# Optimization experiments

Hardware: AMD Instinct MI355X
Metric: run time of the kernel (lower is better)

## Reference

```python
import jax, jax.numpy as jnp
import numpy as np

N_G, N_U, E, C = 100000, 100000, 3200000, 2000000


def graph_conv(x, edges, W_rel, W_root, b):
    # PyG GraphConv (aggr='add'): out_i = (sum_{j->i} x_j) @ W_rel + x_i @ W_root + b
    src, dst = edges[0], edges[1]
    agg = jax.ops.segment_sum(x[src], dst, num_segments=x.shape[0])
    return agg @ W_rel + x @ W_root + b


def setup_inputs() -> dict:
    key = jax.random.key(0)
    ks = jax.random.split(key, 16)
    d = {
        'x_u': jax.random.normal(ks[0], (N_U, 4), jnp.float32),
        'x_g': jax.random.normal(ks[1], (N_G, 4), jnp.float32),
        'candidates': jax.random.randint(ks[2], (C, 2), 0, N_G + N_U, jnp.int64),
        'edges': jax.random.randint(ks[3], (2, E), 0, N_G, jnp.int64),
        # GraphConv(4,8)
        'W1_rel': jax.random.normal(ks[4], (4, 8), jnp.float32) * 0.5,
        'W1_root': jax.random.normal(ks[5], (4, 8), jnp.float32) * 0.5,
        'b1': jax.random.normal(ks[6], (8,), jnp.float32) * 0.1,
        # GraphConv(8,16)
        'W2_rel': jax.random.normal(ks[7], (8, 16), jnp.float32) * 0.35,
        'W2_root': jax.random.normal(ks[8], (8, 16), jnp.float32) * 0.35,
        'b2': jax.random.normal(ks[9], (16,), jnp.float32) * 0.1,
        # fc_unconnected: Linear(4,16) (Dropout is identity in eval)
        'W_un': jax.random.normal(ks[10], (4, 16), jnp.float32) * 0.5,
        'b_un': jax.random.normal(ks[11], (16,), jnp.float32) * 0.1,
        # fc: Linear(32,64) -> SELU -> Linear(64,1)
        'W_fc1': jax.random.normal(ks[12], (32, 64), jnp.float32) * 0.18,
        'b_fc1': jax.random.normal(ks[13], (64,), jnp.float32) * 0.1,
        'W_fc2': jax.random.normal(ks[14], (64, 1), jnp.float32) * 0.12,
        'b_fc2': jax.random.normal(ks[15], (1,), jnp.float32) * 0.1,
    }
    return d


def reference(x_u, x_g, candidates, edges,
              W1_rel, W1_root, b1, W2_rel, W2_root, b2,
              W_un, b_un, W_fc1, b_fc1, W_fc2, b_fc2):
    x_unconnected = x_u @ W_un + b_un                      # [N_u, 16]
    h = jax.nn.selu(graph_conv(x_g, edges, W1_rel, W1_root, b1))   # [N_g, 8]
    x_graph = jax.nn.selu(graph_conv(h, edges, W2_rel, W2_root, b2))  # [N_g, 16]
    x_stacked = jnp.concatenate([x_graph, x_unconnected], axis=0)  # [N_g+N_u, 16]
    ec = jnp.concatenate([x_stacked[candidates[:, 0]],
                          x_stacked[candidates[:, 1]]], axis=1)    # [C, 32]
    hidden = jax.nn.selu(ec @ W_fc1 + b_fc1)               # [C, 64]
    out = (hidden @ W_fc2 + b_fc2).squeeze(-1)             # [C]
    return out


if __name__ == '__main__':
    print(reference(**setup_inputs()).shape)
```

## Files before the change

kernel.cpp:

```cpp
#include <hip/hip_runtime.h>
#include <hip/hip_bf16.h>

#define NG 100000
#define NU 100000
#define NE 3200000
#define NC 2000000

#define BSZ 128
#define NBK 782
#define CAP 5120

#define NSUP 61
#define SFB 13
#define SSPAN (SFB * BSZ)
#define SCAP 56320
#define B1CH 4096
#define B2CH 4096

typedef __attribute__((ext_vector_type(8))) short short8;
typedef __attribute__((ext_vector_type(4))) float floatx4;
typedef unsigned short ushortx8 __attribute__((ext_vector_type(8)));

__device__ __forceinline__ float selu_f(float x) {
    const float LAM = 1.0507009873554805f;
    const float ALA = 1.7580993408473766f;
    const float L2E = 1.44269504088896340736f;
    float e = __builtin_amdgcn_exp2f(fminf(x, 0.f) * L2E);
    return fmaf(LAM, fmaxf(x, 0.f), fmaf(ALA, e, -ALA));
}

__device__ __forceinline__ float bfbits2f(unsigned short u) {
    return __uint_as_float(((unsigned)u) << 16);
}

__device__ __forceinline__ unsigned short f2bfbits(float f) {
    union { __hip_bfloat16 h; unsigned short u; } cv;
    cv.h = __float2bfloat16(f);
    return cv.u;
}

__device__ __forceinline__ float ldf(const void* p, int i, int isbf) {
    return isbf ? bfbits2f(((const unsigned short*)p)[i]) : ((const float*)p)[i];
}

__global__ void k_detect(const unsigned int* __restrict__ xw,
                         const unsigned int* __restrict__ cw,
                         const unsigned int* __restrict__ ew,
                         int* __restrict__ flags) {
    if (threadIdx.x != 0 || blockIdx.x != 0) return;
    int nb = 0;
    for (int i = 0; i < 64; ++i) {
        unsigned lo = xw[i] & 0xffffu;
        unsigned e = (lo >> 7) & 0xff;
        if (e >= 112 && e <= 134) ++nb;
    }
    flags[0] = (nb >= 32) ? 1 : 0;
    int cz = 0, ez = 0;
    for (int i = 0; i < 64; ++i) {
        if (cw[2 * i + 1] == 0u) ++cz;
        if (ew[2 * i + 1] == 0u) ++ez;
    }
    flags[1] = (cz >= 48) ? 1 : 0;
    flags[2] = (ez >= 48) ? 1 : 0;
}

__device__ __forceinline__ void ld_edge(const void* edges, long long e, int e64,
                                        int& s, int& d) {
    if (e64) {
        const long long* el = (const long long*)edges;
        s = (int)el[e];
        d = (int)el[NE + e];
    } else {
        const int* ei = (const int*)edges;
        s = ei[e];
        d = ei[NE + e];
    }
}

__global__ __launch_bounds__(256) void k_bin1(const void* __restrict__ edges,
        int* __restrict__ scur, unsigned int* __restrict__ slist,
        const int* __restrict__ flags) {
    __shared__ unsigned int tmp[B1CH];
    __shared__ unsigned char tsup[B1CH];
    __shared__ unsigned int ord[B1CH];
    __shared__ unsigned char osup[B1CH];
    __shared__ int hist[64];
    __shared__ int lstart[64];
    __shared__ int ofs[64];
    __shared__ int gbase[64];

    int tid = threadIdx.x;
    long long base = (long long)blockIdx.x * B1CH;
    int chunk = (int)(NE - base);
    if (chunk > B1CH) chunk = B1CH;
    int e64 = flags[2];

    if (tid < 64) hist[tid] = 0;
    __syncthreads();

    for (int i = 0; i < B1CH / 256; ++i) {
        int idx = i * 256 + tid;
        if (idx < chunk) {
            int s, d;
            ld_edge(edges, base + idx, e64, s, d);
            int sup = d / SSPAN;
            tmp[idx] = ((unsigned)s << 11) | (unsigned)(d - sup * SSPAN);
            tsup[idx] = (unsigned char)sup;
            atomicAdd(&hist[sup], 1);
        }
    }
    __syncthreads();

    if (tid == 0) {
        int run = 0;
        for (int b = 0; b < NSUP; ++b) {
            lstart[b] = run;
            run += hist[b];
        }
    }
    __syncthreads();
    if (tid < NSUP) {
        int c = hist[tid];
        int g = 0;
        if (c > 0) g = atomicAdd(&scur[tid], c);
        gbase[tid] = g;
        ofs[tid] = lstart[tid];
    }
    __syncthreads();

    for (int i = 0; i < B1CH / 256; ++i) {
        int idx = i * 256 + tid;
        if (idx < chunk) {
            int sup = tsup[idx];
            int pos = atomicAdd(&ofs[sup], 1);
            ord[pos] = tmp[idx];
            osup[pos] = (unsigned char)sup;
        }
    }
    __syncthreads();

    for (int i = 0; i < B1CH / 256; ++i) {
        int idx = i * 256 + tid;
        if (idx < chunk) {
            int sup = osup[idx];
            int p = gbase[sup] + (idx - lstart[sup]);
            if (p < SCAP) slist[(long long)sup * SCAP + p] = ord[idx];
        }
    }
}

#define SCH2 ((SCAP + B2CH - 1) / B2CH)

__global__ __launch_bounds__(256) void k_bin2(const int* __restrict__ scur,
        const unsigned int* __restrict__ slist,
        int* __restrict__ gcur, unsigned int* __restrict__ glist) {
    __shared__ unsigned int tmp[B2CH];
    __shared__ unsigned int ord[B2CH];
    __shared__ unsigned char ofid[B2CH];
    __shared__ int hist[16];
    __shared__ int lstart[16];
    __shared__ int ofs[16];
    __shared__ int gbase[16];

    int tid = threadIdx.x;
    int sup = blockIdx.x / SCH2;
    int ch = blockIdx.x % SCH2;
    int scnt = scur[sup];
    if (scnt > SCAP) scnt = SCAP;
    int start = ch * B2CH;
    int cnt = scnt - start;
    if (cnt <= 0) return;
    if (cnt > B2CH) cnt = B2CH;
    const unsigned int* sp = slist + (long long)sup * SCAP + start;

    if (tid < 16) hist[tid] = 0;
    __syncthreads();

    for (int i = 0; i < B2CH / 256; ++i) {
        int idx = i * 256 + tid;
        if (idx < cnt) {
            unsigned u = sp[idx];
            tmp[idx] = u;
            atomicAdd(&hist[(u & 2047) >> 7], 1);
        }
    }
    __syncthreads();

    if (tid == 0) {
        int run = 0;
        for (int b = 0; b < SFB; ++b) {
            lstart[b] = run;
            run += hist[b];
        }
    }
    __syncthreads();
    if (tid < SFB) {
        int c = hist[tid];
        int g = 0;
        int bf = sup * SFB + tid;
        if (c > 0 && bf < NBK) g = atomicAdd(&gcur[bf], c);
        gbase[tid] = g;
        ofs[tid] = lstart[tid];
    }
    __syncthreads();

    for (int i = 0; i < B2CH / 256; ++i) {
        int idx = i * 256 + tid;
        if (idx < cnt) {
            unsigned u = tmp[idx];
            int dl = u & 2047;
            int f = dl >> 7;
            int pos = atomicAdd(&ofs[f], 1);
            ord[pos] = ((u >> 11) << 7) | (unsigned)(dl & 127);
            ofid[pos] = (unsigned char)f;
        }
    }
    __syncthreads();

    for (int i = 0; i < B2CH / 256; ++i) {
        int idx = i * 256 + tid;
        if (idx < cnt) {
            int f = ofid[idx];
            int bf = sup * SFB + f;
            int p = gbase[f] + (idx - lstart[f]);
            if (p < CAP) glist[(long long)bf * CAP + p] = ord[idx];
        }
    }
}

__global__ __launch_bounds__(256) void k_sort(const int* __restrict__ gcur,
        unsigned int* __restrict__ glist,
        int* __restrict__ dstoff, int* __restrict__ ddeg) {
    __shared__ unsigned int tmp[CAP];
    __shared__ unsigned int sorted[CAP];
    __shared__ int hist[BSZ];
    __shared__ int incl[BSZ];
    __shared__ int cur[BSZ];
    int b = blockIdx.x;
    int tid = threadIdx.x;
    int cnt = gcur[b];
    if (cnt > CAP) cnt = CAP;
    unsigned int* lp = glist + (long long)b * CAP;

    if (tid < BSZ) hist[tid] = 0;
    __syncthreads();
    for (int k = tid; k < cnt; k += 256) {
        unsigned u = lp[k];
        tmp[k] = u;
        atomicAdd(&hist[u & 127], 1);
    }
    __syncthreads();
    if (tid < BSZ) incl[tid] = hist[tid];
    __syncthreads();
    for (int off = 1; off < BSZ; off <<= 1) {
        int v = (tid < BSZ && tid >= off) ? incl[tid - off] : 0;
        __syncthreads();
        if (tid < BSZ && tid >= off) incl[tid] += v;
        __syncthreads();
    }
    if (tid < BSZ) {
        int excl = incl[tid] - hist[tid];
        cur[tid] = excl;
        int d = b * BSZ + tid;
        if (d < NG) {
            dstoff[d] = b * CAP + excl;
            ddeg[d] = hist[tid];
        }
    }
    __syncthreads();
    for (int k = tid; k < cnt; k += 256) {
        unsigned u = tmp[k];
        int pos = atomicAdd(&cur[u & 127], 1);
        sorted[pos] = u >> 7;
    }
    __syncthreads();
    for (int k = tid; k < cnt; k += 256) lp[k] = sorted[k];
}

__global__ __launch_bounds__(256) void k_gather1(const int* __restrict__ dstoff,
        const int* __restrict__ ddeg, const unsigned int* __restrict__ glist,
        const void* __restrict__ xg,
        const void* __restrict__ W1r, const void* __restrict__ W1o,
        const void* __restrict__ b1, unsigned short* __restrict__ hbf,
        const int* __restrict__ flags) {
    int gid = blockIdx.x * 256 + threadIdx.x;
    int d = gid >> 4;
    if (d >= NG) return;
    int q = gid & 15;
    int isbf = flags[0];
    int start = dstoff[d];
    int deg = ddeg[d];
    float a0 = 0.f, a1 = 0.f, a2 = 0.f, a3 = 0.f;
    int k = q;
    for (; k + 16 < deg; k += 32) {
        int s0 = glist[start + k];
        int s1 = glist[start + k + 16];
        if (isbf) {
            ushort4 r0 = *(const ushort4*)((const unsigned short*)xg + s0 * 4);
            ushort4 r1 = *(const ushort4*)((const unsigned short*)xg + s1 * 4);
            a0 += bfbits2f(r0.x) + bfbits2f(r1.x);
            a1 += bfbits2f(r0.y) + bfbits2f(r1.y);
            a2 += bfbits2f(r0.z) + bfbits2f(r1.z);
            a3 += bfbits2f(r0.w) + bfbits2f(r1.w);
        } else {
            float4 r0 = *(const float4*)((const float*)xg + s0 * 4);
            float4 r1 = *(const float4*)((const float*)xg + s1 * 4);
            a0 += r0.x + r1.x;
            a1 += r0.y + r1.y;
            a2 += r0.z + r1.z;
            a3 += r0.w + r1.w;
        }
    }
    for (; k < deg; k += 16) {
        int s = glist[start + k];
        if (isbf) {
            ushort4 r = *(const ushort4*)((const unsigned short*)xg + s * 4);
            a0 += bfbits2f(r.x); a1 += bfbits2f(r.y);
            a2 += bfbits2f(r.z); a3 += bfbits2f(r.w);
        } else {
            float4 r = *(const float4*)((const float*)xg + s * 4);
            a0 += r.x; a1 += r.y; a2 += r.z; a3 += r.w;
        }
    }
#pragma unroll
    for (int off = 1; off < 16; off <<= 1) {
        a0 += __shfl_xor(a0, off);
        a1 += __shfl_xor(a1, off);
        a2 += __shfl_xor(a2, off);
        a3 += __shfl_xor(a3, off);
    }
    if (q < 8) {
        float a[4] = {a0, a1, a2, a3};
        float v = ldf(b1, q, isbf);
#pragma unroll
        for (int c = 0; c < 4; ++c)
            v += a[c] * ldf(W1r, c * 8 + q, isbf)
               + ldf(xg, d * 4 + c, isbf) * ldf(W1o, c * 8 + q, isbf);
        hbf[d * 8 + q] = f2bfbits(selu_f(v));
    }
}

__global__ __launch_bounds__(256) void k_gather2(const int* __restrict__ dstoff,
        const int* __restrict__ ddeg, const unsigned int* __restrict__ glist,
        const ushortx8* __restrict__ hbf,
        const void* __restrict__ W2r, const void* __restrict__ W2o,
        const void* __restrict__ b2, unsigned short* __restrict__ xs,
        const int* __restrict__ flags) {
    int gid = blockIdx.x * 256 + threadIdx.x;
    int d = gid >> 4;
    if (d >= NG) return;
    int q = gid & 15;
    int isbf = flags[0];
    int start = dstoff[d];
    int deg = ddeg[d];
    float a[8] = {0.f, 0.f, 0.f, 0.f, 0.f, 0.f, 0.f, 0.f};
    int k = q;
    for (; k + 16 < deg; k += 32) {
        int s0 = glist[start + k];
        int s1 = glist[start + k + 16];
        ushortx8 r0 = hbf[s0];
        ushortx8 r1 = hbf[s1];
#pragma unroll
        for (int c = 0; c < 8; ++c)
            a[c] += bfbits2f((unsigned short)r0[c]) + bfbits2f((unsigned short)r1[c]);
    }
    for (; k < deg; k += 16) {
        int s = glist[start + k];
        ushortx8 r = hbf[s];
#pragma unroll
        for (int c = 0; c < 8; ++c) a[c] += bfbits2f((unsigned short)r[c]);
    }
#pragma unroll
    for (int off = 1; off < 16; off <<= 1) {
#pragma unroll
        for (int c = 0; c < 8; ++c) a[c] += __shfl_xor(a[c], off);
    }
    ushortx8 hr = hbf[d];
    float hv[8];
#pragma unroll
    for (int c = 0; c < 8; ++c) hv[c] = bfbits2f((unsigned short)hr[c]);
    float v = ldf(b2, q, isbf);
#pragma unroll
    for (int c = 0; c < 8; ++c)
        v += a[c] * ldf(W2r, c * 16 + q, isbf)
           + hv[c] * ldf(W2o, c * 16 + q, isbf);
    xs[d * 16 + q] = f2bfbits(selu_f(v));
}

__global__ __launch_bounds__(256) void k_unconn(const void* __restrict__ xu,
        const void* __restrict__ Wun, const void* __restrict__ bun,
        unsigned short* __restrict__ xs, const int* __restrict__ flags) {
    int u = blockIdx.x * 256 + threadIdx.x;
    if (u >= NU) return;
    int isbf = flags[0];
    float x[4];
#pragma unroll
    for (int k = 0; k < 4; ++k) x[k] = ldf(xu, u * 4 + k, isbf);
    ushortx8 lo, hi;
#pragma unroll
    for (int j = 0; j < 16; ++j) {
        float v = ldf(bun, j, isbf);
#pragma unroll
        for (int k = 0; k < 4; ++k)
            v += x[k] * ldf(Wun, k * 16 + j, isbf);
        unsigned short bb = f2bfbits(v);
        if (j < 8) lo[j] = bb; else hi[j - 8] = bb;
    }
    ushortx8* xp = (ushortx8*)(xs + (NG + u) * 16);
    xp[0] = lo;
    xp[1] = hi;
}

__device__ __forceinline__ int2 ld_cand2(const void* cand, int c, int c64) {
    if (c64) {
        const long long* cl = (const long long*)cand;
        return make_int2((int)cl[2 * c], (int)cl[2 * c + 1]);
    }
    return *(const int2*)((const int*)cand + 2 * c);
}

__global__ __launch_bounds__(256) void k_fc(const unsigned short* __restrict__ xs,
        const void* __restrict__ cand,
        const void* __restrict__ Wfc1, const void* __restrict__ bfc1,
        const void* __restrict__ Wfc2, const void* __restrict__ bfc2,
        void* __restrict__ out, const int* __restrict__ flags) {
    int lane = threadIdx.x & 63;
    int wid = (blockIdx.x * blockDim.x + threadIdx.x) >> 6;
    int m = lane & 15;
    int half = lane >> 4;
    int isbf = flags[0], c64 = flags[1];

    short8 bfrag[4];
#pragma unroll
    for (int t = 0; t < 4; ++t) {
#pragma unroll
        for (int j = 0; j < 8; ++j)
            bfrag[t][j] = (short)f2bfbits(ldf(Wfc1, (half * 8 + j) * 64 + t * 16 + m, isbf));
    }
    float bias[4], w2v[4];
#pragma unroll
    for (int t = 0; t < 4; ++t) {
        bias[t] = ldf(bfc1, t * 16 + m, isbf);
        w2v[t] = ldf(Wfc2, t * 16 + m, isbf);
    }
    float b2s = ldf(bfc2, 0, isbf);
    floatx4 zero = {0.f, 0.f, 0.f, 0.f};

    const int nTiles = NC / 16;
    int nW = (gridDim.x * blockDim.x) >> 6;
    if (wid >= nTiles) return;

    int tn1 = wid + nW;
    int2 cc_cur = ld_cand2(cand, wid * 16 + m, c64);
    int tn1c = (tn1 < nTiles) ? tn1 : wid;
    int2 cc_nxt = ld_cand2(cand, tn1c * 16 + m, c64);
    {
        int row = (half < 2) ? cc_cur.x : cc_cur.y;
        short8 af_cur = *(const short8*)(xs + row * 16 + (half & 1) * 8);

        for (int t = wid; t < nTiles; t += nW) {
            int tnn = t + 2 * nW;
            int tnnc = (tnn < nTiles) ? tnn : t;
            int2 cc_n2 = ld_cand2(cand, tnnc * 16 + m, c64);
            int rown = (half < 2) ? cc_nxt.x : cc_nxt.y;
            short8 af_nxt = *(const short8*)(xs + rown * 16 + (half & 1) * 8);

            float part[4] = {0.f, 0.f, 0.f, 0.f};
#pragma unroll
            for (int tt = 0; tt < 4; ++tt) {
                floatx4 ac = __builtin_amdgcn_mfma_f32_16x16x32_bf16(af_cur, bfrag[tt], zero, 0, 0, 0);
#pragma unroll
                for (int r = 0; r < 4; ++r) {
                    float hvv = selu_f(ac[r] + bias[tt]);
                    part[r] = fmaf(hvv, w2v[tt], part[r]);
                }
            }
#pragma unroll
            for (int off = 1; off < 16; off <<= 1) {
#pragma unroll
                for (int r = 0; r < 4; ++r)
                    part[r] += __shfl_xor(part[r], off, 64);
            }
            if (m == 0) {
                if (isbf) {
                    ushort4 o;
                    o.x = f2bfbits(part[0] + b2s);
                    o.y = f2bfbits(part[1] + b2s);
                    o.z = f2bfbits(part[2] + b2s);
                    o.w = f2bfbits(part[3] + b2s);
                    *(ushort4*)((unsigned short*)out + t * 16 + half * 4) = o;
                } else {
                    float4 o = make_float4(part[0] + b2s, part[1] + b2s,
                                           part[2] + b2s, part[3] + b2s);
                    *(float4*)((float*)out + t * 16 + half * 4) = o;
                }
            }
            cc_nxt = cc_n2;
            af_cur = af_nxt;
        }
    }
}

extern "C" void kernel_launch(void* const* d_in, const int* in_sizes, int n_in,
                              void* d_out, int out_size, void* d_ws, size_t ws_size,
                              hipStream_t stream) {
    const void* x_u = d_in[0];
    const void* x_g = d_in[1];
    const void* cand = d_in[2];
    const void* edges = d_in[3];
    const void* W1r = d_in[4];
    const void* W1o = d_in[5];
    const void* b1 = d_in[6];
    const void* W2r = d_in[7];
    const void* W2o = d_in[8];
    const void* b2 = d_in[9];
    const void* Wun = d_in[10];
    const void* bun = d_in[11];
    const void* Wfc1 = d_in[12];
    const void* bfc1 = d_in[13];
    const void* Wfc2 = d_in[14];
    const void* bfc2 = d_in[15];

    char* ws = (char*)d_ws;
    int* flags = (int*)ws;
    int* gcur = (int*)(ws + 64);
    int* scur = (int*)(ws + 3264);
    unsigned int* glist = (unsigned int*)(ws + 4160);
    size_t glist_bytes = (size_t)NBK * CAP * 4;
    char* p = ws + 4160 + glist_bytes;
    unsigned int* slist = (unsigned int*)p;
    int* dstoff = (int*)p;
    int* ddeg = (int*)(p + 400000);
    unsigned short* hbf = (unsigned short*)(p + 800000);
    unsigned short* xs = (unsigned short*)(p + 2400000);

    hipMemsetAsync(gcur, 0, 3456, stream);

    k_detect<<<1, 64, 0, stream>>>((const unsigned int*)x_u,
                                   (const unsigned int*)cand,
                                   (const unsigned int*)edges, flags);
    k_bin1<<<(NE + B1CH - 1) / B1CH, 256, 0, stream>>>(edges, scur, slist, flags);
    k_bin2<<<NSUP * SCH2, 256, 0, stream>>>(scur, slist, gcur, glist);
    k_sort<<<NBK, 256, 0, stream>>>(gcur, glist, dstoff, ddeg);
    k_gather1<<<(16 * NG + 255) / 256, 256, 0, stream>>>(dstoff, ddeg, glist, x_g,
                                                         W1r, W1o, b1, hbf, flags);
    k_gather2<<<(16 * NG + 255) / 256, 256, 0, stream>>>(dstoff, ddeg, glist,
                                                         (const ushortx8*)hbf,
                                                         W2r, W2o, b2, xs, flags);
    k_unconn<<<(NU + 255) / 256, 256, 0, stream>>>(x_u, Wun, bun, xs, flags);
    k_fc<<<2048, 256, 0, stream>>>(xs, cand, Wfc1, bfc1, Wfc2, bfc2, d_out, flags);
}
```

Before: 280.3 us.

## Transpose FC MFMA, fold bias into accumulator, and simplify SELU reduction

Swaps the MFMA operands so each lane holds hidden units for one candidate. That reduces the per-candidate sum over the 64 hidden units to two cross-lane shuffles instead of four shuffle rounds on four values. The fc1 bias is passed as the MFMA accumulator input, and SELU is rewritten branch-free as lam*max(v,0) + alpha*lam*exp(min(v,0)). The constant -alpha*lam*sum(w2) is folded into the output bias. This trims per-element ALU work, but the exp is now computed for every element and the floating-point rounding changes slightly.

Result: no change. 280.7 us (+0.1%).

```diff
diff --git a/kernel.cpp b/kernel.cpp
--- a/kernel.cpp
+++ b/kernel.cpp
@@ -424,27 +424,38 @@
         const void* __restrict__ Wfc1, const void* __restrict__ bfc1,
         const void* __restrict__ Wfc2, const void* __restrict__ bfc2,
         void* __restrict__ out, const int* __restrict__ flags) {
+    const float LAM = 1.0507009873554805f;
+    const float ALA = 1.7580993408473766f;
+    const float L2E = 1.44269504088896340736f;
     int lane = threadIdx.x & 63;
     int wid = (blockIdx.x * blockDim.x + threadIdx.x) >> 6;
     int m = lane & 15;
     int half = lane >> 4;
     int isbf = flags[0], c64 = flags[1];
 
-    short8 bfrag[4];
+    short8 wfrag[4];
 #pragma unroll
     for (int t = 0; t < 4; ++t) {
 #pragma unroll
         for (int j = 0; j < 8; ++j)
-            bfrag[t][j] = (short)f2bfbits(ldf(Wfc1, (half * 8 + j) * 64 + t * 16 + m, isbf));
-    }
-    float bias[4], w2v[4];
+            wfrag[t][j] = (short)f2bfbits(ldf(Wfc1, (half * 8 + j) * 64 + t * 16 + m, isbf));
+    }
+    floatx4 cbias[4];
+    float w2L[4][4], w2A[4][4];
 #pragma unroll
     for (int t = 0; t < 4; ++t) {
-        bias[t] = ldf(bfc1, t * 16 + m, isbf);
-        w2v[t] = ldf(Wfc2, t * 16 + m, isbf);
-    }
-    float b2s = ldf(bfc2, 0, isbf);
-    floatx4 zero = {0.f, 0.f, 0.f, 0.f};
+#pragma unroll
+        for (int r = 0; r < 4; ++r) {
+            int h = t * 16 + half * 4 + r;
+            cbias[t][r] = ldf(bfc1, h, isbf);
+            float w2 = ldf(Wfc2, h, isbf);
+            w2L[t][r] = w2 * LAM;
+            w2A[t][r] = w2 * ALA;
+        }
+    }
+    float sumw2 = 0.f;
+    for (int h = 0; h < 64; ++h) sumw2 += ldf(Wfc2, h, isbf);
+    float c_corr = ldf(bfc2, 0, isbf) - ALA * sumw2;
 
     const int nTiles = NC / 16;
     int nW = (gridDim.x * blockDim.x) >> 6;
@@ -465,35 +476,25 @@
             int rown = (half < 2) ? cc_nxt.x : cc_nxt.y;
             short8 af_nxt = *(const short8*)(xs + rown * 16 + (half & 1) * 8);
 
-            float part[4] = {0.f, 0.f, 0.f, 0.f};
+            float part = 0.f;
 #pragma unroll
             for (int tt = 0; tt < 4; ++tt) {
-                floatx4 ac = __builtin_amdgcn_mfma_f32_16x16x32_bf16(af_cur, bfrag[tt], zero, 0, 0, 0);
+                floatx4 ac = __builtin_amdgcn_mfma_f32_16x16x32_bf16(
+                    wfrag[tt], af_cur, cbias[tt], 0, 0, 0);
 #pragma unroll
                 for (int r = 0; r < 4; ++r) {
-                    float hvv = selu_f(ac[r] + bias[tt]);
-                    part[r] = fmaf(hvv, w2v[tt], part[r]);
+                    float v = ac[r];
+                    float e = __builtin_amdgcn_exp2f(fminf(v, 0.f) * L2E);
+                    part = fmaf(w2L[tt][r], fmaxf(v, 0.f), part);
+                    part = fmaf(w2A[tt][r], e, part);
                 }
             }
-#pragma unroll
-            for (int off = 1; off < 16; off <<= 1) {
-#pragma unroll
-                for (int r = 0; r < 4; ++r)
-                    part[r] += __shfl_xor(part[r], off, 64);
-            }
-            if (m == 0) {
-                if (isbf) {
-                    ushort4 o;
-                    o.x = f2bfbits(part[0] + b2s);
-                    o.y = f2bfbits(part[1] + b2s);
-                    o.z = f2bfbits(part[2] + b2s);
-                    o.w = f2bfbits(part[3] + b2s);
-                    *(ushort4*)((unsigned short*)out + t * 16 + half * 4) = o;
-                } else {
-                    float4 o = make_float4(part[0] + b2s, part[1] + b2s,
-                                           part[2] + b2s, part[3] + b2s);
-                    *(float4*)((float*)out + t * 16 + half * 4) = o;
-                }
+            part += __shfl_xor(part, 16, 64);
+            part += __shfl_xor(part, 32, 64);
+            if (half == 0) {
+                float o = part + c_corr;
+                if (isbf) ((unsigned short*)out)[t * 16 + m] = f2bfbits(o);
+                else ((float*)out)[t * 16 + m] = o;
             }
             cc_nxt = cc_n2;
             af_cur = af_nxt;
```
